# Performance work log

Hardware: AMD Instinct MI355X
Metric: run time of the kernel (lower is better)

Reference implementation:

```python
import jax, jax.numpy as jnp
import numpy as np

B = 65536
N_SPARSE = 20
N_VARLEN = 3
SEQ_LEN = 50
VOCAB = 100000
N_DENSE = 13


def setup_inputs() -> dict:
    key = jax.random.key(0)
    k1, k2, k3, k4, k5, k6 = jax.random.split(key, 6)
    sparse_ids = jax.random.randint(k1, (B, N_SPARSE), 0, VOCAB, dtype=jnp.int64 if jax.config.jax_enable_x64 else jnp.int32)
    varlen_ids = jax.random.randint(k2, (B, N_VARLEN, SEQ_LEN), 0, VOCAB, dtype=sparse_ids.dtype)
    dense_x = jax.random.normal(k3, (B, N_DENSE), dtype=jnp.float32)
    # dim-1 embedding table per feature, stacked: [n_feat, vocab]
    sparse_tables = jax.random.normal(k4, (N_SPARSE, VOCAB), dtype=jnp.float32)
    varlen_tables = jax.random.normal(k5, (N_VARLEN, VOCAB), dtype=jnp.float32)
    dense_w = jax.random.normal(k6, (N_DENSE,), dtype=jnp.float32) * 1e-4
    return {
        "sparse_ids": sparse_ids,
        "varlen_ids": varlen_ids,
        "dense_x": dense_x,
        "sparse_tables": sparse_tables,
        "varlen_tables": varlen_tables,
        "dense_w": dense_w,
    }


def reference(sparse_ids, varlen_ids, dense_x, sparse_tables, varlen_tables, dense_w):
    # per-feature dim-1 embedding gather for single-value sparse feats: [B, Fs]
    fs = jnp.arange(N_SPARSE)
    sparse_vals = sparse_tables[fs[None, :], sparse_ids]
    # varlen gather: [B, Fv, L]; mask_zero=True -> id 0 contributes nothing; sum pooling
    fv = jnp.arange(N_VARLEN)
    varlen_vals = varlen_tables[fv[None, :, None], varlen_ids]
    mask = (varlen_ids != 0).astype(varlen_vals.dtype)
    varlen_pool = jnp.sum(varlen_vals * mask, axis=-1)  # [B, Fv]
    # reduce_sum over concat([sparse_vals, varlen_pool]) == sum of both sums
    logit = jnp.sum(sparse_vals, axis=-1) + jnp.sum(varlen_pool, axis=-1)
    # linear dense logit: concat(dense) @ W[:,1], squeezed
    logit = logit + dense_x @ dense_w
    return logit  # [B]
```

## Files before the change

### kernel.cpp

```cpp
#include <hip/hip_runtime.h>

constexpr int B        = 65536;
constexpr int N_SPARSE = 20;
constexpr int N_VARLEN = 3;
constexpr int SEQ_LEN  = 50;
constexpr int VOCAB    = 100000;
constexpr int N_DENSE  = 13;
constexpr int VAR_TOT  = N_VARLEN * SEQ_LEN;

__global__ __launch_bounds__(256) void logit_kernel(
    const int*   __restrict__ sparse_ids,
    const int*   __restrict__ varlen_ids,
    const float* __restrict__ dense_x,
    const float* __restrict__ sparse_tables,
    const float* __restrict__ varlen_tables,
    const float* __restrict__ dense_w,
    float*       __restrict__ out)
{
    const int tid = blockIdx.x * blockDim.x + threadIdx.x;
    const int row = tid >> 2;
    const int t   = tid & 3;
    if (row >= B) return;

    float acc0 = 0.f, acc1 = 0.f;

    const int* srow = sparse_ids + (long)row * N_SPARSE;
    int sid[5];
    #pragma unroll
    for (int i = 0; i < 5; ++i) sid[i] = srow[t + 4 * i];
    #pragma unroll
    for (int i = 0; i < 5; ++i) {
        const int f = t + 4 * i;
        acc0 += sparse_tables[f * VOCAB + sid[i]];
    }

    const int* vrow = varlen_ids + (long)row * VAR_TOT;
    {
        int p = t;
        while (p + 28 < VAR_TOT) {
            int id[8];
            #pragma unroll
            for (int i = 0; i < 8; ++i) id[i] = vrow[p + 4 * i];
            #pragma unroll
            for (int i = 0; i < 8; ++i) {
                const int pp = p + 4 * i;
                const int v  = (pp >= 100) ? 2 : (pp >= 50 ? 1 : 0);
                const float val = varlen_tables[v * VOCAB + id[i]];
                if (i & 1) acc1 += (id[i] != 0) ? val : 0.f;
                else       acc0 += (id[i] != 0) ? val : 0.f;
            }
            p += 32;
        }
        for (; p < VAR_TOT; p += 4) {
            const int id = vrow[p];
            const int v  = (p >= 100) ? 2 : (p >= 50 ? 1 : 0);
            const float val = varlen_tables[v * VOCAB + id];
            acc0 += (id != 0) ? val : 0.f;
        }
    }

    const float* drow = dense_x + (long)row * N_DENSE;
    #pragma unroll
    for (int d = t; d < N_DENSE; d += 4)
        acc1 += drow[d] * dense_w[d];

    float acc = acc0 + acc1;
    acc += __shfl_xor(acc, 1);
    acc += __shfl_xor(acc, 2);
    if (t == 0) out[row] = acc;
}

extern "C" void kernel_launch(void* const* d_in, const int* in_sizes, int n_in,
                              void* d_out, int out_size, void* d_ws, size_t ws_size,
                              hipStream_t stream) {
    const int*   sparse_ids    = (const int*)d_in[0];
    const int*   varlen_ids    = (const int*)d_in[1];
    const float* dense_x       = (const float*)d_in[2];
    const float* sparse_tables = (const float*)d_in[3];
    const float* varlen_tables = (const float*)d_in[4];
    const float* dense_w       = (const float*)d_in[5];
    float*       out           = (float*)d_out;

    const int threads = 256;
    const int total   = B * 4;
    const int blocks  = (total + threads - 1) / threads;
    logit_kernel<<<blocks, threads, 0, stream>>>(
        sparse_ids, varlen_ids, dense_x, sparse_tables, varlen_tables, dense_w, out);
}
```

Measured before the change: 141.4 us.

## Process row pairs with 16 lanes using 128-bit vectorized id loads

Each group of 16 threads now handles two consecutive rows, loading their varlen ids, sparse ids and dense features as int4/float2 vectors so global reads are wide and coalesced. Per-element row membership is computed from the flat index, with two accumulators and a 16-lane shuffle reduction, and both results are written as one float2. The aim is to cut load instruction count and improve coalescing of the id streams. In exchange it adds per-element select logic, a longer reduction, and the layout assumes B is even and that row-pair strides are 16-byte aligned.

Measured after the change: 136.9 us. 1.03x faster.

```diff
diff --git a/kernel.cpp b/kernel.cpp
--- a/kernel.cpp
+++ b/kernel.cpp
@@ -18,56 +18,87 @@
     float*       __restrict__ out)
 {
     const int tid = blockIdx.x * blockDim.x + threadIdx.x;
-    const int row = tid >> 2;
-    const int t   = tid & 3;
-    if (row >= B) return;
+    const int g   = tid >> 4;
+    const int t   = tid & 15;
+
+    const int4*   vptr = (const int4*)(varlen_ids) + (long)g * 75;
+    const int4*   sptr = (const int4*)(sparse_ids) + (long)g * 10;
+    const float2* dptr = (const float2*)(dense_x)  + (long)g * 13;
+
+    int4 vid[5];
+    #pragma unroll
+    for (int k = 0; k < 4; ++k) vid[k] = vptr[t + 16 * k];
+    const bool v5 = (t + 64) < 75;
+    if (v5) vid[4] = vptr[t + 64];
+
+    int4 sid;
+    const bool hs = (t < 10);
+    if (hs) sid = sptr[t];
+
+    float2 dx;
+    const bool hd = (t < 13);
+    if (hd) dx = dptr[t];
 
     float acc0 = 0.f, acc1 = 0.f;
 
-    const int* srow = sparse_ids + (long)row * N_SPARSE;
-    int sid[5];
     #pragma unroll
-    for (int i = 0; i < 5; ++i) sid[i] = srow[t + 4 * i];
-    #pragma unroll
-    for (int i = 0; i < 5; ++i) {
-        const int f = t + 4 * i;
-        acc0 += sparse_tables[f * VOCAB + sid[i]];
-    }
-
-    const int* vrow = varlen_ids + (long)row * VAR_TOT;
-    {
-        int p = t;
-        while (p + 28 < VAR_TOT) {
-            int id[8];
-            #pragma unroll
-            for (int i = 0; i < 8; ++i) id[i] = vrow[p + 4 * i];
-            #pragma unroll
-            for (int i = 0; i < 8; ++i) {
-                const int pp = p + 4 * i;
-                const int v  = (pp >= 100) ? 2 : (pp >= 50 ? 1 : 0);
-                const float val = varlen_tables[v * VOCAB + id[i]];
-                if (i & 1) acc1 += (id[i] != 0) ? val : 0.f;
-                else       acc0 += (id[i] != 0) ? val : 0.f;
-            }
-            p += 32;
-        }
-        for (; p < VAR_TOT; p += 4) {
-            const int id = vrow[p];
+    for (int k = 0; k < 5; ++k) {
+        if (k == 4 && !v5) continue;
+        const int s0 = 4 * (t + 16 * k);
+        const int ids[4] = { vid[k].x, vid[k].y, vid[k].z, vid[k].w };
+        #pragma unroll
+        for (int j = 0; j < 4; ++j) {
+            const int s  = s0 + j;
+            const bool r1 = (s >= VAR_TOT);
+            const int p  = r1 ? (s - VAR_TOT) : s;
             const int v  = (p >= 100) ? 2 : (p >= 50 ? 1 : 0);
-            const float val = varlen_tables[v * VOCAB + id];
-            acc0 += (id != 0) ? val : 0.f;
+            const float val = varlen_tables[v * VOCAB + ids[j]];
+            const float m   = (ids[j] != 0) ? val : 0.f;
+            acc0 += r1 ? 0.f : m;
+            acc1 += r1 ? m   : 0.f;
         }
     }
 
-    const float* drow = dense_x + (long)row * N_DENSE;
+    if (hs) {
+        const int s0 = 4 * t;
+        const int ids[4] = { sid.x, sid.y, sid.z, sid.w };
+        #pragma unroll
+        for (int j = 0; j < 4; ++j) {
+            const int s  = s0 + j;
+            const bool r1 = (s >= N_SPARSE);
+            const int f  = r1 ? (s - N_SPARSE) : s;
+            const float val = sparse_tables[f * VOCAB + ids[j]];
+            acc0 += r1 ? 0.f : val;
+            acc1 += r1 ? val : 0.f;
+        }
+    }
+
+    if (hd) {
+        const int s0 = 2 * t;
+        {
+            const int s = s0;
+            const bool r1 = (s >= N_DENSE);
+            const int d = r1 ? (s - N_DENSE) : s;
+            const float prod = dx.x * dense_w[d];
+            acc0 += r1 ? 0.f : prod;
+            acc1 += r1 ? prod : 0.f;
+        }
+        {
+            const int s = s0 + 1;
+            const bool r1 = (s >= N_DENSE);
+            const int d = r1 ? (s - N_DENSE) : s;
+            const float prod = dx.y * dense_w[d];
+            acc0 += r1 ? 0.f : prod;
+            acc1 += r1 ? prod : 0.f;
+        }
+    }
+
     #pragma unroll
-    for (int d = t; d < N_DENSE; d += 4)
-        acc1 += drow[d] * dense_w[d];
-
-    float acc = acc0 + acc1;
-    acc += __shfl_xor(acc, 1);
-    acc += __shfl_xor(acc, 2);
-    if (t == 0) out[row] = acc;
+    for (int o = 1; o < 16; o <<= 1) {
+        acc0 += __shfl_xor(acc0, o);
+        acc1 += __shfl_xor(acc1, o);
+    }
+    if (t == 0) ((float2*)out)[g] = make_float2(acc0, acc1);
 }
 
 extern "C" void kernel_launch(void* const* d_in, const int* in_sizes, int n_in,
@@ -82,8 +113,8 @@
     float*       out           = (float*)d_out;
 
     const int threads = 256;
-    const int total   = B * 4;
-    const int blocks  = (total + threads - 1) / threads;
+    const int total   = (B / 2) * 16;
+    const int blocks  = total / threads;
     logit_kernel<<<blocks, threads, 0, stream>>>(
         sparse_ids, varlen_ids, dense_x, sparse_tables, varlen_tables, dense_w, out);
 }
```
